# Kernel optimization log

Measured on AMD Instinct MI355X. Metric: run time of the kernel, lower is better.

The kernel has to match this reference:

```python
import jax, jax.numpy as jnp
import numpy as np

N, E, T, F = 20000, 320000, 64, 16
HG, HT = 128, 256


def setup_inputs() -> dict:
    key = jax.random.key(0)
    ks = jax.random.split(key, 18)
    s = 0.05
    p = lambda k, shape: jax.random.normal(k, shape, jnp.float32) * s
    return {
        "x_seq": jax.random.normal(ks[0], (1, T, N, F), jnp.float32),
        "edge_index": jax.random.randint(ks[1], (2, E), 0, N, jnp.int32),
        # SAGEConv 1 (PyG default: mean aggregation; lin_l on aggregated neighbors w/ bias, lin_r on root w/o bias)
        "W1l": p(ks[2], (HG, F)), "b1l": p(ks[3], (HG,)), "W1r": p(ks[4], (HG, F)),
        # SAGEConv 2
        "W2l": p(ks[5], (HG, HG)), "b2l": p(ks[6], (HG,)), "W2r": p(ks[7], (HG, HG)),
        # GRU (torch gate order: r, z, n)
        "W_ih": p(ks[8], (3 * HT, HG)), "W_hh": p(ks[9], (3 * HT, HT)),
        "b_ih": p(ks[10], (3 * HT,)), "b_hh": p(ks[11], (3 * HT,)),
        # head: Linear(HT,64) -> ReLU -> Linear(64,1)
        "Wh1": p(ks[12], (64, HT)), "bh1": p(ks[13], (64,)),
        "Wh2": p(ks[14], (1, 64)), "bh2": p(ks[15], (1,)),
    }


def reference(x_seq, edge_index, W1l, b1l, W1r, W2l, b2l, W2r,
              W_ih, W_hh, b_ih, b_hh, Wh1, bh1, Wh2, bh2):
    n_nodes = x_seq.shape[2]
    src, dst = edge_index[0], edge_index[1]
    # in-degree for mean aggregation (0 -> output 0, matching scatter-mean)
    deg = jax.ops.segment_sum(jnp.ones(src.shape[0], x_seq.dtype), dst,
                              num_segments=n_nodes)
    inv_deg = jnp.where(deg > 0, 1.0 / deg, 0.0)[:, None]  # [N,1]

    def sage(x, Wl, bl, Wr):
        # mean over incoming neighbor messages, then linear + root linear
        agg = jax.ops.segment_sum(x[src], dst, num_segments=n_nodes) * inv_deg
        return agg @ Wl.T + bl + x @ Wr.T

    def graph_step(carry, x_t):  # x_t: [N, F]
        h = jax.nn.relu(sage(x_t, W1l, b1l, W1r))
        h = jax.nn.relu(sage(h, W2l, b2l, W2r))
        return carry, h.mean(axis=0)  # [HG]

    _, Hg = jax.lax.scan(graph_step, 0, x_seq[0])  # [T, HG]

    hidden_t = W_hh.shape[1]

    def gru_step(h, x_t):
        gi = x_t @ W_ih.T + b_ih
        gh = h @ W_hh.T + b_hh
        i_r, i_z, i_n = jnp.split(gi, 3)
        h_r, h_z, h_n = jnp.split(gh, 3)
        r = jax.nn.sigmoid(i_r + h_r)
        z = jax.nn.sigmoid(i_z + h_z)
        n = jnp.tanh(i_n + r * h_n)
        h_new = (1.0 - z) * n + z * h
        return h_new, h_new

    h0 = jnp.zeros((hidden_t,), x_seq.dtype)
    h_last, _ = jax.lax.scan(gru_step, h0, Hg)  # [HT]

    y = jax.nn.relu(h_last @ Wh1.T + bh1) @ Wh2.T + bh2  # [1]
    return y
```

## Files before the change

kernel.cpp:

```cpp
#include <hip/hip_runtime.h>
#include <hip/hip_bf16.h>

#define N_NODES 20000
#define N_EDGES 320000
#define T_STEPS 64
#define F_IN    16
#define HGd     128
#define HTd     256
#define INVN    (1.0f/20000.0f)
#define NTILES   625
#define S1T      79
#define NG64     313
#define QSCALE   64.0f
#define INVQ     (1.0f/64.0f)
#define QX       32.0f
#define INVQX    (1.0f/32.0f)
#define S_Q8     ((size_t)(N_NODES + 1) * HGd)

typedef __attribute__((ext_vector_type(8))) short short8;
typedef __attribute__((ext_vector_type(4))) float f32x4;
typedef __attribute__((ext_vector_type(2))) float f32x2;
typedef __attribute__((ext_vector_type(2))) _Float16 half2t;

static __device__ __forceinline__ ushort f2bf(float f) {
    __hip_bfloat16 b = __float2bfloat16(f);
    return *reinterpret_cast<ushort*>(&b);
}
static __device__ __forceinline__ half2t u2h(uint u) {
    half2t h; __builtin_memcpy(&h, &u, 4); return h;
}
static __device__ __forceinline__ uint packf16(float a, float b) {
    auto h = __builtin_amdgcn_cvt_pkrtz(a, b);
    uint u; __builtin_memcpy(&u, &h, 4); return u;
}

__global__ void k_zero(int* __restrict__ deg, float* __restrict__ HgP,
                       int* __restrict__ jobc, int* __restrict__ bins,
                       uint* __restrict__ h1q, int tch) {
    int i = blockIdx.x * blockDim.x + threadIdx.x;
    if (i < N_NODES) deg[i] = 0;
    if (i < T_STEPS * 8 * HGd) HgP[i] = 0.0f;
    if (i < 1024) jobc[i] = 0;
    if (i < 256) bins[i] = 0;
    if (i < tch * 32) {
        int sl = i >> 5, j = i & 31;
        h1q[sl * (S_Q8 / 4) + (size_t)N_NODES * (HGd / 4) + j] = 0u;
    }
}

__global__ void k_degree(const int* __restrict__ ei, int* __restrict__ deg) {
    int e = blockIdx.x * blockDim.x + threadIdx.x;
    if (e < N_EDGES) atomicAdd(&deg[ei[N_EDGES + e]], 1);
}

__global__ __launch_bounds__(1024) void k_scan(const int* __restrict__ deg,
        int* __restrict__ rp, int* __restrict__ cursor, float* __restrict__ invd) {
    __shared__ int sh[1024];
    __shared__ int carry_s;
    int tid = threadIdx.x;
    if (tid == 0) { carry_s = 0; rp[0] = 0; }
    __syncthreads();
    for (int base = 0; base < N_NODES; base += 1024) {
        int i = base + tid;
        int v = (i < N_NODES) ? deg[i] : 0;
        sh[tid] = v;
        __syncthreads();
        for (int off = 1; off < 1024; off <<= 1) {
            int t = (tid >= off) ? sh[tid - off] : 0;
            __syncthreads();
            sh[tid] += t;
            __syncthreads();
        }
        int inc = sh[tid] + carry_s;
        if (i < N_NODES) {
            rp[i + 1] = inc;
            cursor[i] = inc - v;
            invd[i] = (v > 0) ? (1.0f / (float)v) : 0.0f;
        }
        __syncthreads();
        if (tid == 1023) carry_s = inc;
        __syncthreads();
    }
}

__global__ void k_fill(const int* __restrict__ ei, int* __restrict__ cursor,
                       int* __restrict__ csr) {
    int e = blockIdx.x * blockDim.x + threadIdx.x;
    if (e < N_EDGES) {
        int d = ei[N_EDGES + e];
        int p = atomicAdd(&cursor[d], 1);
        csr[p] = ei[e];
    }
}

__global__ void k_hist(const int* __restrict__ deg, int* __restrict__ bins) {
    int i = blockIdx.x * blockDim.x + threadIdx.x;
    if (i < N_NODES) atomicAdd(&bins[min(deg[i], 255)], 1);
}

__global__ __launch_bounds__(256) void k_binscan(const int* __restrict__ bins,
        int* __restrict__ bincur, int* __restrict__ nodebefore,
        int* __restrict__ edgebefore, int* __restrict__ edgebp, int* __restrict__ rp2p) {
    __shared__ int sh[256], she[256], shp[256];
    int tid = threadIdx.x;
    int b = bins[tid];
    int dp = (tid + 7) & ~7;
    sh[tid] = b;
    she[tid] = b * tid;
    shp[tid] = b * dp;
    __syncthreads();
    for (int off = 1; off < 256; off <<= 1) {
        int v = (tid >= off) ? sh[tid - off] : 0;
        int ve = (tid >= off) ? she[tid - off] : 0;
        int vp = (tid >= off) ? shp[tid - off] : 0;
        __syncthreads();
        sh[tid] += v; she[tid] += ve; shp[tid] += vp;
        __syncthreads();
    }
    bincur[tid] = sh[tid] - b;
    nodebefore[tid] = sh[tid] - b;
    edgebefore[tid] = she[tid] - b * tid;
    edgebp[tid] = shp[tid] - b * dp;
    if (tid == 255) rp2p[N_NODES] = shp[255];
}

__global__ void k_perm(const int* __restrict__ deg, int* __restrict__ bincur,
                       const int* __restrict__ nodebefore, const int* __restrict__ edgebefore,
                       const int* __restrict__ edgebp, const float* __restrict__ invd,
                       int* __restrict__ perm, int* __restrict__ pos,
                       int* __restrict__ rp2, float* __restrict__ invd2,
                       int* __restrict__ degs2, int* __restrict__ rp2p) {
    int i = blockIdx.x * blockDim.x + threadIdx.x;
    if (i < N_NODES) {
        int d = min(deg[i], 255);
        int p = atomicAdd(&bincur[d], 1);
        int rank = p - nodebefore[d];
        perm[p] = i;
        pos[i] = p;
        rp2[p] = edgebefore[d] + rank * d;
        rp2p[p] = edgebp[d] + rank * ((d + 7) & ~7);
        invd2[p] = invd[i];
        degs2[p] = deg[i];
        if (i == 0) rp2[N_NODES] = N_EDGES;
    }
}

__global__ __launch_bounds__(512) void k_tb(const int* __restrict__ rp2, int* __restrict__ tb) {
    __shared__ int sh[512];
    int t = threadIdx.x;
    int md = 0;
    if (t < NG64 && t * 64 < N_NODES) {
        int last = min((t + 1) * 64, N_NODES) - 1;
        md = rp2[last + 1] - rp2[last];
    }
    sh[t] = 64 * md;
    __syncthreads();
    for (int off = 1; off < 512; off <<= 1) {
        int v = (t >= off) ? sh[t - off] : 0;
        __syncthreads();
        sh[t] += v;
        __syncthreads();
    }
    tb[t + 1] = sh[t];
    if (t == 0) tb[0] = 0;
}

__global__ void k_ecopy(const int* __restrict__ rp, const int* __restrict__ pos,
                        const int* __restrict__ rp2p, const int* __restrict__ tb,
                        const int* __restrict__ csr,
                        int* __restrict__ csr3, int* __restrict__ csr2p) {
    int e = blockIdx.x * blockDim.x + threadIdx.x;
    if (e < N_EDGES) {
        int lo = 0, hi = N_NODES - 1;
#pragma unroll
        for (int it = 0; it < 15; ++it) {
            int mid = (lo + hi + 1) >> 1;
            if (rp[mid] <= e) lo = mid; else hi = mid - 1;
        }
        int i = lo;
        int j = e - rp[i];
        int p = pos[i];
        int v = csr[e];
        csr3[tb[p >> 6] + j * 64 + (p & 63)] = v;
        csr2p[rp2p[p] + j] = v;
    }
}

__global__ void k_pad(const int* __restrict__ rp, const int* __restrict__ pos,
                      const int* __restrict__ rp2p, int* __restrict__ csr2p) {
    int i = blockIdx.x * blockDim.x + threadIdx.x;
    if (i < N_NODES) {
        int d = rp[i + 1] - rp[i];
        int dp = (d + 7) & ~7;
        int o = rp2p[pos[i]];
        for (int k = d; k < dp; ++k) csr2p[o + k] = N_NODES;
    }
}

__global__ void k_qx(const float* __restrict__ xs, int* __restrict__ x8, int n4) {
    int i = blockIdx.x * blockDim.x + threadIdx.x;
    if (i < n4) {
        float4 v = reinterpret_cast<const float4*>(xs)[i];
        int q8 = __builtin_amdgcn_cvt_pk_fp8_f32(v.x * QX, v.y * QX, 0, false);
        q8 = __builtin_amdgcn_cvt_pk_fp8_f32(v.z * QX, v.w * QX, q8, true);
        x8[i] = q8;
    }
}

__global__ void k_prepw(const float* __restrict__ W1l, const float* __restrict__ W1r,
                        const float* __restrict__ W2l, const float* __restrict__ W2r,
                        const float* __restrict__ W_ih, const float* __restrict__ W_hh,
                        ushort* __restrict__ W1T2, ushort* __restrict__ WT2,
                        float* __restrict__ WihT, uint* __restrict__ W_hhq) {
    int i = blockIdx.x * blockDim.x + threadIdx.x;
    const int n1 = 128 * 32, n2 = 128 * 256, n3 = 128 * 768, n4 = 128 * 768;
    if (i < n1) {
        int o = i >> 5, k = i & 31;
        float v = (k < 16) ? W1l[o * 16 + k] : W1r[o * 16 + (k - 16)];
        W1T2[i] = f2bf(v);
    } else if (i < n1 + n2) {
        int j = i - n1; int o = j >> 8, k = j & 255;
        float v = (k < 128) ? W2l[o * 128 + k] : W2r[o * 128 + (k - 128)];
        WT2[j] = f2bf(v);
    } else if (i < n1 + n2 + n3) {
        int j = i - n1 - n2; int k = j / 768, g = j % 768;
        WihT[j] = W_ih[g * 128 + k];
    } else if (i < n1 + n2 + n3 + n4) {
        int j = i - n1 - n2 - n3; int dw = j / 768, row = j % 768;
        float a = W_hh[(size_t)row * HTd + 2 * dw];
        float b = W_hh[(size_t)row * HTd + 2 * dw + 1];
        W_hhq[j] = packf16(a, b);
    }
}

__global__ __launch_bounds__(256) void k_sage1(
        const char* __restrict__ x8_, const int* __restrict__ tb,
        const int* __restrict__ csr3, const int* __restrict__ degs2,
        const float* __restrict__ invd2,
        const ushort* __restrict__ W1T2, const float* __restrict__ b1l,
        const int* __restrict__ perm, uchar1* __restrict__ h1q_,
        int* __restrict__ jobc, int C) {
    __shared__ ushort u[256 * 40];
    __shared__ int pnode[256];
    __shared__ int job_s;
    int tid = threadIdx.x;
    int l = tid & 63, w = tid >> 6;
    int lane15 = l & 15, g4 = l >> 4;
    const int xcd = blockIdx.x & 7;
    const int cmin = (C < 8) ? C : 8;
    const int ci = xcd % cmin;
    const int reps = (C >= 8) ? (C >> 3) : 1;
    int* ctr = jobc + ci;
    const int njobs = reps * S1T;

    short8 bfr1[2];
    float bb1[2];
#pragma unroll
    for (int ct = 0; ct < 2; ++ct) {
        int o16 = w * 32 + ct * 16 + lane15;
        bfr1[ct] = *reinterpret_cast<const short8*>(W1T2 + o16 * 32 + g4 * 8);
        bb1[ct] = b1l[o16];
    }

    for (;;) {
        if (tid == 0) job_s = atomicAdd(ctr, 1);
        __syncthreads();
        int job = job_s;
        if (job >= njobs) break;
        int rep = job / S1T;
        int tile = job - rep * S1T;
        int tl = ci + (rep << 3);
        const char* xq = x8_ + (size_t)tl * N_NODES * F_IN;
        char* h1q = (char*)h1q_ + (size_t)tl * S_Q8;
        int p = tile * 256 + tid;
        int node = (p < N_NODES) ? perm[p] : -1;
        pnode[tid] = node;

        float acc[16], rootv[16];
#pragma unroll
        for (int k = 0; k < 16; ++k) { acc[k] = 0.0f; rootv[k] = 0.0f; }
        if (node >= 0) {
            int d = degs2[p];
            const int base = tb[p >> 6] + (p & 63);
            for (int j = 0; j < d; ++j) {
                int idx = csr3[base + j * 64];
                uint4 row = *reinterpret_cast<const uint4*>(xq + (size_t)idx * F_IN);
#pragma unroll
                for (int c = 0; c < 4; ++c) {
                    uint vd = c == 0 ? row.x : c == 1 ? row.y : c == 2 ? row.z : row.w;
                    f32x2 lo = __builtin_amdgcn_cvt_pk_f32_fp8((int)vd, false);
                    f32x2 hi = __builtin_amdgcn_cvt_pk_f32_fp8((int)vd, true);
                    acc[4 * c + 0] += lo.x; acc[4 * c + 1] += lo.y;
                    acc[4 * c + 2] += hi.x; acc[4 * c + 3] += hi.y;
                }
            }
            float id = invd2[p] * INVQX;
#pragma unroll
            for (int k = 0; k < 16; ++k) acc[k] *= id;
            uint4 rv = *reinterpret_cast<const uint4*>(xq + (size_t)node * F_IN);
#pragma unroll
            for (int c = 0; c < 4; ++c) {
                uint vd = c == 0 ? rv.x : c == 1 ? rv.y : c == 2 ? rv.z : rv.w;
                f32x2 lo = __builtin_amdgcn_cvt_pk_f32_fp8((int)vd, false);
                f32x2 hi = __builtin_amdgcn_cvt_pk_f32_fp8((int)vd, true);
                rootv[4 * c + 0] = lo.x * INVQX; rootv[4 * c + 1] = lo.y * INVQX;
                rootv[4 * c + 2] = hi.x * INVQX; rootv[4 * c + 3] = hi.y * INVQX;
            }
        }
        {
            uint dw[16];
#pragma unroll
            for (int i = 0; i < 8; ++i)
                dw[i] = (uint)f2bf(acc[2 * i]) | ((uint)f2bf(acc[2 * i + 1]) << 16);
#pragma unroll
            for (int i = 0; i < 8; ++i)
                dw[8 + i] = (uint)f2bf(rootv[2 * i]) | ((uint)f2bf(rootv[2 * i + 1]) << 16);
            ushort* ur = u + tid * 40;
#pragma unroll
            for (int c = 0; c < 4; ++c)
                *reinterpret_cast<uint4*>(ur + c * 8) =
                    make_uint4(dw[4 * c], dw[4 * c + 1], dw[4 * c + 2], dw[4 * c + 3]);
        }
        __syncthreads();

#pragma unroll 4
        for (int rt = 0; rt < 16; ++rt) {
            int row = rt * 16 + lane15;
            short8 af = *reinterpret_cast<const short8*>(u + row * 40 + g4 * 8);
            f32x4 a0 = __builtin_amdgcn_mfma_f32_16x16x32_bf16(af, bfr1[0], (f32x4)(0.0f), 0, 0, 0);
            f32x4 a1 = __builtin_amdgcn_mfma_f32_16x16x32_bf16(af, bfr1[1], (f32x4)(0.0f), 0, 0, 0);
#pragma unroll
            for (int j = 0; j < 4; ++j) {
                int nl = rt * 16 + g4 * 4 + j;
                int nd = pnode[nl];
                if (nd >= 0) {
                    float v0 = fmaxf(a0[j] + bb1[0], 0.0f) * QSCALE;
                    float v1 = fmaxf(a1[j] + bb1[1], 0.0f) * QSCALE;
                    int q0 = __builtin_amdgcn_cvt_pk_fp8_f32(v0, v0, 0, false);
                    int q1 = __builtin_amdgcn_cvt_pk_fp8_f32(v1, v1, 0, false);
                    h1q[(size_t)nd * HGd + w * 32 + lane15] = (char)q0;
                    h1q[(size_t)nd * HGd + w * 32 + 16 + lane15] = (char)q1;
                }
            }
        }
    }
}

__global__ __launch_bounds__(256) void k_sage2(
        const uchar1* __restrict__ h1q_,
        const int* __restrict__ rp2p, const int* __restrict__ csr2p,
        const float* __restrict__ invd2,
        const ushort* __restrict__ WT2, const float* __restrict__ b2l,
        const int* __restrict__ perm, float* __restrict__ HgP,
        int* __restrict__ jobc, int t0, int C) {
    __shared__ uint4 usm4[32 * 512 / 16];
    __shared__ int pnode[32];
    __shared__ int job_s;
    char* ub = (char*)usm4;
    int tid = threadIdx.x;
    int l = tid & 63, w = tid >> 6;
    int lane15 = l & 15, g4 = l >> 4;
    int sub = (l >> 3) & 1, seg8 = l & 7;
    const int xcd = blockIdx.x & 7;
    const int cmin = (C < 8) ? C : 8;
    const int ci = xcd % cmin;
    const int reps = (C >= 8) ? (C >> 3) : 1;
    int* ctr = jobc + ci;
    const int njobs = reps * NTILES;

    short8 bfr[2][8];
    float bb[2];
#pragma unroll
    for (int ct = 0; ct < 2; ++ct) {
        int n = w * 32 + ct * 16 + lane15;
        const ushort* bp = WT2 + n * 256 + g4 * 8;
#pragma unroll
        for (int ks = 0; ks < 8; ++ks)
            bfr[ct][ks] = *reinterpret_cast<const short8*>(bp + ks * 32);
        bb[ct] = b2l[n];
    }

    for (;;) {
        if (tid == 0) job_s = atomicAdd(ctr, 1);
        __syncthreads();
        int job = job_s;
        if (job >= njobs) break;
        int rep = job / NTILES;
        int tile = job - rep * NTILES;
        int tl = ci + ((reps - 1 - rep) << 3);
        int t = t0 + tl;
        const char* h1q = (const char*)h1q_ + (size_t)tl * S_Q8;
        int nbase = tile * 32;
        if (tid < 32) pnode[tid] = perm[nbase + tid];
        __syncthreads();

        {
            int nl = tid >> 3, seg = tid & 7;
            uint4 v = *reinterpret_cast<const uint4*>(h1q + (size_t)pnode[nl] * HGd + seg * 16);
            uint bw[8];
#pragma unroll
            for (int d = 0; d < 4; ++d) {
                uint vd = d == 0 ? v.x : d == 1 ? v.y : d == 2 ? v.z : v.w;
                f32x2 plo = __builtin_amdgcn_cvt_pk_f32_fp8((int)vd, false);
                f32x2 phi = __builtin_amdgcn_cvt_pk_f32_fp8((int)vd, true);
                bw[2 * d]     = (uint)f2bf(plo.x * INVQ) | ((uint)f2bf(plo.y * INVQ) << 16);
                bw[2 * d + 1] = (uint)f2bf(phi.x * INVQ) | ((uint)f2bf(phi.y * INVQ) << 16);
            }
            int base = nl * 512 + 256 + seg * 32;
            int swz = (nl & 7) << 4;
            *reinterpret_cast<uint4*>(ub + (base ^ swz)) =
                make_uint4(bw[0], bw[1], bw[2], bw[3]);
            *reinterpret_cast<uint4*>(ub + ((base + 16) ^ swz)) =
                make_uint4(bw[4], bw[5], bw[6], bw[7]);
        }

#pragma unroll
        for (int g = 0; g < 2; ++g) {
            int nl = w * 8 + g * 4 + g4;
            int sl = rp2p[nbase + nl];
            int dp = rp2p[nbase + nl + 1] - sl;
            const int* cp = csr2p + sl;
            float af[16];
#pragma unroll
            for (int k = 0; k < 16; ++k) af[k] = 0.0f;
            if (dp > 0) {
                int idx[4];
#pragma unroll
                for (int uu = 0; uu < 4; ++uu) idx[uu] = cp[2 * uu + sub];
                for (int j = 0; j < dp; j += 8) {
                    uint4 vv[4];
#pragma unroll
                    for (int uu = 0; uu < 4; ++uu)
                        vv[uu] = *reinterpret_cast<const uint4*>(h1q + (size_t)idx[uu] * HGd + seg8 * 16);
                    cp += 8;
#pragma unroll
                    for (int uu = 0; uu < 4; ++uu) idx[uu] = cp[2 * uu + sub];
#pragma unroll
                    for (int uu = 0; uu < 4; ++uu) {
#pragma unroll
                        for (int c = 0; c < 4; ++c) {
                            uint vd = c == 0 ? vv[uu].x : c == 1 ? vv[uu].y
                                     : c == 2 ? vv[uu].z : vv[uu].w;
                            f32x2 lo = __builtin_amdgcn_cvt_pk_f32_fp8((int)vd, false);
                            f32x2 hi = __builtin_amdgcn_cvt_pk_f32_fp8((int)vd, true);
                            af[4 * c + 0] += lo.x; af[4 * c + 1] += lo.y;
                            af[4 * c + 2] += hi.x; af[4 * c + 3] += hi.y;
                        }
                    }
                }
            }
#pragma unroll
            for (int k = 0; k < 16; ++k) af[k] += __shfl_xor(af[k], 8);
            float id = invd2[nbase + nl] * INVQ;
            if (sub == 0) {
                uint bw[8];
#pragma unroll
                for (int i2 = 0; i2 < 8; ++i2)
                    bw[i2] = (uint)f2bf(af[2 * i2] * id) |
                             ((uint)f2bf(af[2 * i2 + 1] * id) << 16);
                int base = nl * 512 + seg8 * 32;
                int swz = (nl & 7) << 4;
                *reinterpret_cast<uint4*>(ub + (base ^ swz)) =
                    make_uint4(bw[0], bw[1], bw[2], bw[3]);
                *reinterpret_cast<uint4*>(ub + ((base + 16) ^ swz)) =
                    make_uint4(bw[4], bw[5], bw[6], bw[7]);
            }
        }
        __syncthreads();

        f32x4 acc[2][2];
#pragma unroll
        for (int rt = 0; rt < 2; ++rt)
#pragma unroll
            for (int ct = 0; ct < 2; ++ct) acc[rt][ct] = (f32x4)(0.0f);
#pragma unroll
        for (int ks = 0; ks < 8; ++ks) {
#pragma unroll
            for (int rt = 0; rt < 2; ++rt) {
                int row = rt * 16 + lane15;
                int byt = (row * 512 + (ks * 32 + g4 * 8) * 2) ^ ((row & 7) << 4);
                short8 af = *reinterpret_cast<const short8*>(ub + byt);
                acc[rt][0] = __builtin_amdgcn_mfma_f32_16x16x32_bf16(af, bfr[0][ks], acc[rt][0], 0, 0, 0);
                acc[rt][1] = __builtin_amdgcn_mfma_f32_16x16x32_bf16(af, bfr[1][ks], acc[rt][1], 0, 0, 0);
            }
        }
#pragma unroll
        for (int ct = 0; ct < 2; ++ct) {
            float sum = 0.f;
#pragma unroll
            for (int rt = 0; rt < 2; ++rt)
#pragma unroll
                for (int j = 0; j < 4; ++j)
                    sum += fmaxf(acc[rt][ct][j] + bb[ct], 0.f);
            sum += __shfl_xor(sum, 16);
            sum += __shfl_xor(sum, 32);
            if (g4 == 0) {
                int n = w * 32 + ct * 16 + lane15;
                atomicAdd(&HgP[(t * 8 + (tile & 7)) * HGd + n], sum);
            }
        }
    }
}

__global__ __launch_bounds__(768) void k_gi(const float* __restrict__ HgP,
        const float* __restrict__ WihT, const float* __restrict__ b_ih,
        float* __restrict__ gi_all) {
    __shared__ float x[HGd];
    int t = blockIdx.x, g = threadIdx.x;
    if (g < HGd) {
        float s = 0.f;
#pragma unroll
        for (int p = 0; p < 8; ++p) s += HgP[(t * 8 + p) * HGd + g];
        x[g] = s * INVN;
    }
    __syncthreads();
    float a = b_ih[g];
    for (int k = 0; k < HGd; ++k) a += WihT[k * 768 + g] * x[k];
    gi_all[t * 768 + g] = a;
}

__global__ __launch_bounds__(768, 3) void k_gru1b(const float* __restrict__ gi_all,
        const uint* __restrict__ W_hhq, const float* __restrict__ b_hh,
        const float* __restrict__ Wh1, const float* __restrict__ bh1,
        const float* __restrict__ Wh2, const float* __restrict__ bh2,
        float* __restrict__ out) {
    int tid = threadIdx.x;
    uint wv[128];
#pragma unroll
    for (int i = 0; i < 128; ++i) wv[i] = W_hhq[i * 768 + tid];
    float bh = b_hh[tid];

    __shared__ float hs[HTd];
    __shared__ uint h2s[HTd / 2];
    __shared__ float gh[3 * HTd];
    if (tid < HTd) hs[tid] = 0.0f;
    if (tid < HTd / 2) h2s[tid] = 0u;
    __syncthreads();

    for (int t = 0; t < T_STEPS; ++t) {
        float s = bh;
#pragma unroll
        for (int i = 0; i < 128; i += 4) {
            uint4 hh = *reinterpret_cast<const uint4*>(&h2s[i]);
            s = __builtin_amdgcn_fdot2(u2h(wv[i + 0]), u2h(hh.x), s, false);
            s = __builtin_amdgcn_fdot2(u2h(wv[i + 1]), u2h(hh.y), s, false);
            s = __builtin_amdgcn_fdot2(u2h(wv[i + 2]), u2h(hh.z), s, false);
            s = __builtin_amdgcn_fdot2(u2h(wv[i + 3]), u2h(hh.w), s, false);
        }
        gh[tid] = s;
        __syncthreads();
        if (tid < HTd) {
            float gir = gi_all[t * 768 + tid];
            float giz = gi_all[t * 768 + HTd + tid];
            float gin = gi_all[t * 768 + 2 * HTd + tid];
            float r = 1.0f / (1.0f + expf(-(gir + gh[tid])));
            float z = 1.0f / (1.0f + expf(-(giz + gh[HTd + tid])));
            float n = tanhf(gin + r * gh[2 * HTd + tid]);
            hs[tid] = (1.0f - z) * n + z * hs[tid];
        }
        __syncthreads();
        if (tid < HTd / 2)
            h2s[tid] = packf16(hs[2 * tid], hs[2 * tid + 1]);
        __syncthreads();
    }

    __shared__ float act[64];
    if (tid < 64) {
        float a = bh1[tid];
        const float* wr = Wh1 + tid * HTd;
        for (int k = 0; k < HTd; k += 4) {
            float4 wv4 = *reinterpret_cast<const float4*>(wr + k);
            a += wv4.x * hs[k] + wv4.y * hs[k + 1] + wv4.z * hs[k + 2] + wv4.w * hs[k + 3];
        }
        act[tid] = fmaxf(a, 0.0f);
    }
    __syncthreads();
    if (tid == 0) {
        float y = bh2[0];
        for (int j = 0; j < 64; ++j) y += Wh2[j] * act[j];
        out[0] = y;
    }
}

extern "C" void kernel_launch(void* const* d_in, const int* in_sizes, int n_in,
                              void* d_out, int out_size, void* d_ws, size_t ws_size,
                              hipStream_t stream) {
    const float* x_seq = (const float*)d_in[0];
    const int*   ei    = (const int*)d_in[1];
    const float* W1l   = (const float*)d_in[2];
    const float* b1l   = (const float*)d_in[3];
    const float* W1r   = (const float*)d_in[4];
    const float* W2l   = (const float*)d_in[5];
    const float* b2l   = (const float*)d_in[6];
    const float* W2r   = (const float*)d_in[7];
    const float* W_ih  = (const float*)d_in[8];
    const float* W_hh  = (const float*)d_in[9];
    const float* b_ih  = (const float*)d_in[10];
    const float* b_hh  = (const float*)d_in[11];
    const float* Wh1   = (const float*)d_in[12];
    const float* bh1   = (const float*)d_in[13];
    const float* Wh2   = (const float*)d_in[14];
    const float* bh2   = (const float*)d_in[15];
    float* out = (float*)d_out;

    char* ws = (char*)d_ws;
    size_t off = 0;
    auto take = [&](size_t nbytes) -> void* {
        void* p = (void*)(ws + off);
        off += (nbytes + 255) & ~(size_t)255;
        return p;
    };
    int*    deg    = (int*)take(N_NODES * 4);
    int*    rp     = (int*)take((N_NODES + 1) * 4);
    int*    cursor = (int*)take(N_NODES * 4);
    int*    csr    = (int*)take(N_EDGES * 4);
    float*  invd   = (float*)take(N_NODES * 4);
    int*    perm   = (int*)take(N_NODES * 4);
    int*    pos    = (int*)take(N_NODES * 4);
    int*    rp2    = (int*)take((N_NODES + 2) * 4);
    int*    rp2p   = (int*)take((N_NODES + 2) * 4);
    int*    csr2p  = (int*)take(480300 * 4);
    float*  invd2  = (float*)take(N_NODES * 4);
    int*    degs2  = (int*)take(N_NODES * 4);
    int*    tb     = (int*)take(520 * 4);
    int*    csr3   = (int*)take(360000 * 4);
    int*    bins   = (int*)take(256 * 4);
    int*    bincur = (int*)take(256 * 4);
    int*    nodeb  = (int*)take(256 * 4);
    int*    edgeb  = (int*)take(256 * 4);
    int*    edgebp = (int*)take(256 * 4);
    ushort* W1T2   = (ushort*)take(128 * 32 * 2);
    ushort* WT2    = (ushort*)take(128 * 256 * 2);
    float*  WihT   = (float*)take(128 * 768 * 4);
    uint*   W_hhq  = (uint*)take(128 * 768 * 4);
    float*  HgP    = (float*)take(T_STEPS * 8 * HGd * 4);
    float*  gi_all = (float*)take(T_STEPS * 768 * 4);
    int*    jobc   = (int*)take(1024 * 4);

    const size_t slice_q = (S_Q8 + 255) & ~(size_t)255;
    const size_t slice_x = ((size_t)N_NODES * F_IN + 255) & ~(size_t)255;
    int T_CH = 64;
    while (T_CH > 1 && off + (size_t)T_CH * (slice_q + slice_x) > ws_size)
        T_CH >>= 1;
    uchar1* h1q = (uchar1*)take((size_t)T_CH * slice_q);
    char*   x8  = (char*)take((size_t)T_CH * slice_x);

    k_zero<<<256, 256, 0, stream>>>(deg, HgP, jobc, bins, (uint*)h1q, T_CH);
    k_degree<<<(N_EDGES + 255) / 256, 256, 0, stream>>>(ei, deg);
    k_scan<<<1, 1024, 0, stream>>>(deg, rp, cursor, invd);
    k_fill<<<(N_EDGES + 255) / 256, 256, 0, stream>>>(ei, cursor, csr);
    k_hist<<<(N_NODES + 255) / 256, 256, 0, stream>>>(deg, bins);
    k_binscan<<<1, 256, 0, stream>>>(bins, bincur, nodeb, edgeb, edgebp, rp2p);
    k_perm<<<(N_NODES + 255) / 256, 256, 0, stream>>>(deg, bincur, nodeb, edgeb, edgebp,
                                                      invd, perm, pos, rp2, invd2, degs2, rp2p);
    k_tb<<<1, 512, 0, stream>>>(rp2, tb);
    k_ecopy<<<(N_EDGES + 255) / 256, 256, 0, stream>>>(rp, pos, rp2p, tb, csr, csr3, csr2p);
    k_pad<<<(N_NODES + 255) / 256, 256, 0, stream>>>(rp, pos, rp2p, csr2p);
    {
        int total = 128 * 32 + 128 * 256 + 128 * 768 + 128 * 768;
        k_prepw<<<(total + 255) / 256, 256, 0, stream>>>(W1l, W1r, W2l, W2r, W_ih, W_hh,
                                                         W1T2, WT2, WihT, W_hhq);
    }
    int chunk = 0;
    for (int t0 = 0; t0 < T_STEPS; t0 += T_CH, ++chunk) {
        int C = T_CH;
        int n4 = C * N_NODES * F_IN / 4;
        k_qx<<<(n4 + 255) / 256, 256, 0, stream>>>(
            x_seq + (size_t)t0 * N_NODES * F_IN, (int*)x8, n4);
        k_sage1<<<2048, 256, 0, stream>>>(x8, tb, csr3, degs2, invd2, W1T2, b1l, perm,
                                          h1q, jobc + chunk * 32, C);
        k_sage2<<<2048, 256, 0, stream>>>(h1q, rp2p, csr2p, invd2, WT2, b2l, perm, HgP,
                                          jobc + chunk * 32 + 16, t0, C);
    }
    k_gi<<<T_STEPS, 768, 0, stream>>>(HgP, WihT, b_ih, gi_all);
    k_gru1b<<<1, 768, 0, stream>>>(gi_all, W_hhq, b_hh, Wh1, bh1, Wh2, bh2, out);
}
```

Baseline: 999.5 us.

## Switch SAGE2 gather and MFMA from bf16/fp32 to packed fp16

After: 999.4 us. Within noise of the previous version (-0.0%).

```diff
diff --git a/kernel.cpp b/kernel.cpp
--- a/kernel.cpp
+++ b/kernel.cpp
@@ -29,9 +29,23 @@
 static __device__ __forceinline__ half2t u2h(uint u) {
     half2t h; __builtin_memcpy(&h, &u, 4); return h;
 }
+static __device__ __forceinline__ uint h2u(half2t h) {
+    uint u; __builtin_memcpy(&u, &h, 4); return u;
+}
 static __device__ __forceinline__ uint packf16(float a, float b) {
     auto h = __builtin_amdgcn_cvt_pkrtz(a, b);
     uint u; __builtin_memcpy(&u, &h, 4); return u;
+}
+static __device__ __forceinline__ ushort f2h(float a) {
+    return (ushort)(packf16(a, a) & 0xffffu);
+}
+static __device__ __forceinline__ half2t cvt8h_lo(uint v) {
+    auto h = __builtin_amdgcn_cvt_scalef32_pk_f16_fp8(v, 1.0f, false);
+    half2t r; __builtin_memcpy(&r, &h, 4); return r;
+}
+static __device__ __forceinline__ half2t cvt8h_hi(uint v) {
+    auto h = __builtin_amdgcn_cvt_scalef32_pk_f16_fp8(v, 1.0f, true);
+    half2t r; __builtin_memcpy(&r, &h, 4); return r;
 }
 
 __global__ void k_zero(int* __restrict__ deg, float* __restrict__ HgP,
@@ -210,7 +224,7 @@
 __global__ void k_prepw(const float* __restrict__ W1l, const float* __restrict__ W1r,
                         const float* __restrict__ W2l, const float* __restrict__ W2r,
                         const float* __restrict__ W_ih, const float* __restrict__ W_hh,
-                        ushort* __restrict__ W1T2, ushort* __restrict__ WT2,
+                        ushort* __restrict__ W1T2, ushort* __restrict__ WT2f,
                         float* __restrict__ WihT, uint* __restrict__ W_hhq) {
     int i = blockIdx.x * blockDim.x + threadIdx.x;
     const int n1 = 128 * 32, n2 = 128 * 256, n3 = 128 * 768, n4 = 128 * 768;
@@ -221,7 +235,7 @@
     } else if (i < n1 + n2) {
         int j = i - n1; int o = j >> 8, k = j & 255;
         float v = (k < 128) ? W2l[o * 128 + k] : W2r[o * 128 + (k - 128)];
-        WT2[j] = f2bf(v);
+        WT2f[j] = f2h(v * INVQ);
     } else if (i < n1 + n2 + n3) {
         int j = i - n1 - n2; int k = j / 768, g = j % 768;
         WihT[j] = W_ih[g * 128 + k];
@@ -350,7 +364,7 @@
         const uchar1* __restrict__ h1q_,
         const int* __restrict__ rp2p, const int* __restrict__ csr2p,
         const float* __restrict__ invd2,
-        const ushort* __restrict__ WT2, const float* __restrict__ b2l,
+        const ushort* __restrict__ WT2f, const float* __restrict__ b2l,
         const int* __restrict__ perm, float* __restrict__ HgP,
         int* __restrict__ jobc, int t0, int C) {
     __shared__ uint4 usm4[32 * 512 / 16];
@@ -373,7 +387,7 @@
 #pragma unroll
     for (int ct = 0; ct < 2; ++ct) {
         int n = w * 32 + ct * 16 + lane15;
-        const ushort* bp = WT2 + n * 256 + g4 * 8;
+        const ushort* bp = WT2f + n * 256 + g4 * 8;
 #pragma unroll
         for (int ks = 0; ks < 8; ++ks)
             bfr[ct][ks] = *reinterpret_cast<const short8*>(bp + ks * 32);
@@ -401,10 +415,8 @@
 #pragma unroll
             for (int d = 0; d < 4; ++d) {
                 uint vd = d == 0 ? v.x : d == 1 ? v.y : d == 2 ? v.z : v.w;
-                f32x2 plo = __builtin_amdgcn_cvt_pk_f32_fp8((int)vd, false);
-                f32x2 phi = __builtin_amdgcn_cvt_pk_f32_fp8((int)vd, true);
-                bw[2 * d]     = (uint)f2bf(plo.x * INVQ) | ((uint)f2bf(plo.y * INVQ) << 16);
-                bw[2 * d + 1] = (uint)f2bf(phi.x * INVQ) | ((uint)f2bf(phi.y * INVQ) << 16);
+                bw[2 * d]     = h2u(cvt8h_lo(vd));
+                bw[2 * d + 1] = h2u(cvt8h_hi(vd));
             }
             int base = nl * 512 + 256 + seg * 32;
             int swz = (nl & 7) << 4;
@@ -420,9 +432,9 @@
             int sl = rp2p[nbase + nl];
             int dp = rp2p[nbase + nl + 1] - sl;
             const int* cp = csr2p + sl;
-            float af[16];
-#pragma unroll
-            for (int k = 0; k < 16; ++k) af[k] = 0.0f;
+            half2t a[8];
+#pragma unroll
+            for (int k = 0; k < 8; ++k) a[k] = (half2t)0;
             if (dp > 0) {
                 int idx[4];
 #pragma unroll
@@ -441,23 +453,24 @@
                         for (int c = 0; c < 4; ++c) {
                             uint vd = c == 0 ? vv[uu].x : c == 1 ? vv[uu].y
                                      : c == 2 ? vv[uu].z : vv[uu].w;
-                            f32x2 lo = __builtin_amdgcn_cvt_pk_f32_fp8((int)vd, false);
-                            f32x2 hi = __builtin_amdgcn_cvt_pk_f32_fp8((int)vd, true);
-                            af[4 * c + 0] += lo.x; af[4 * c + 1] += lo.y;
-                            af[4 * c + 2] += hi.x; af[4 * c + 3] += hi.y;
+                            a[2 * c]     += cvt8h_lo(vd);
+                            a[2 * c + 1] += cvt8h_hi(vd);
                         }
                     }
                 }
             }
-#pragma unroll
-            for (int k = 0; k < 16; ++k) af[k] += __shfl_xor(af[k], 8);
-            float id = invd2[nbase + nl] * INVQ;
+            float idf = invd2[nbase + nl];
+            _Float16 idh = (_Float16)idf;
+            half2t idv; idv[0] = idh; idv[1] = idh;
+            uint bw[8];
+#pragma unroll
+            for (int k = 0; k < 8; ++k) {
+                uint av = h2u(a[k]);
+                uint ao = __shfl_xor(av, 8);
+                half2t s = (u2h(av) + u2h(ao)) * idv;
+                bw[k] = h2u(s);
+            }
             if (sub == 0) {
-                uint bw[8];
-#pragma unroll
-                for (int i2 = 0; i2 < 8; ++i2)
-                    bw[i2] = (uint)f2bf(af[2 * i2] * id) |
-                             ((uint)f2bf(af[2 * i2 + 1] * id) << 16);
                 int base = nl * 512 + seg8 * 32;
                 int swz = (nl & 7) << 4;
                 *reinterpret_cast<uint4*>(ub + (base ^ swz)) =
@@ -480,8 +493,8 @@
                 int row = rt * 16 + lane15;
                 int byt = (row * 512 + (ks * 32 + g4 * 8) * 2) ^ ((row & 7) << 4);
                 short8 af = *reinterpret_cast<const short8*>(ub + byt);
-                acc[rt][0] = __builtin_amdgcn_mfma_f32_16x16x32_bf16(af, bfr[0][ks], acc[rt][0], 0, 0, 0);
-                acc[rt][1] = __builtin_amdgcn_mfma_f32_16x16x32_bf16(af, bfr[1][ks], acc[rt][1], 0, 0, 0);
+                acc[rt][0] = __builtin_amdgcn_mfma_f32_16x16x32_f16(af, bfr[0][ks], acc[rt][0], 0, 0, 0);
+                acc[rt][1] = __builtin_amdgcn_mfma_f32_16x16x32_f16(af, bfr[1][ks], acc[rt][1], 0, 0, 0);
             }
         }
 #pragma unroll
@@ -630,7 +643,7 @@
     int*    edgeb  = (int*)take(256 * 4);
     int*    edgebp = (int*)take(256 * 4);
     ushort* W1T2   = (ushort*)take(128 * 32 * 2);
-    ushort* WT2    = (ushort*)take(128 * 256 * 2);
+    ushort* WT2f   = (ushort*)take(128 * 256 * 2);
     float*  WihT   = (float*)take(128 * 768 * 4);
     uint*   W_hhq  = (uint*)take(128 * 768 * 4);
     float*  HgP    = (float*)take(T_STEPS * 8 * HGd * 4);
@@ -659,7 +672,7 @@
     {
         int total = 128 * 32 + 128 * 256 + 128 * 768 + 128 * 768;
         k_prepw<<<(total + 255) / 256, 256, 0, stream>>>(W1l, W1r, W2l, W2r, W_ih, W_hh,
-                                                         W1T2, WT2, WihT, W_hhq);
+                                                         W1T2, WT2f, WihT, W_hhq);
     }
     int chunk = 0;
     for (int t0 = 0; t0 < T_STEPS; t0 += T_CH, ++chunk) {
@@ -669,7 +682,7 @@
             x_seq + (size_t)t0 * N_NODES * F_IN, (int*)x8, n4);
         k_sage1<<<2048, 256, 0, stream>>>(x8, tb, csr3, degs2, invd2, W1T2, b1l, perm,
                                           h1q, jobc + chunk * 32, C);
-        k_sage2<<<2048, 256, 0, stream>>>(h1q, rp2p, csr2p, invd2, WT2, b2l, perm, HgP,
+        k_sage2<<<2048, 256, 0, stream>>>(h1q, rp2p, csr2p, invd2, WT2f, b2l, perm, HgP,
                                           jobc + chunk * 32 + 16, t0, C);
     }
     k_gi<<<T_STEPS, 768, 0, stream>>>(HgP, WihT, b_ih, gi_all);
```
